# Optimization experiments

Measured on AMD Instinct MI355X. Metric: run time of the kernel, lower is better.

## Reference

```python
import jax, jax.numpy as jnp
import numpy as np

N = 100000      # nodes
E = 1600000     # edges (before self-loops)
IN = 128        # in_size
H = 4           # heads
C = 32          # out_size // heads
OUT = H * C     # 128
NEG_SLOPE = 0.2
LN_EPS = 1e-5
SM_EPS = 1e-16  # PyG softmax eps


def setup_inputs() -> dict:
    key = jax.random.key(0)
    ks = jax.random.split(key, 6)
    x = jax.random.normal(ks[0], (N, IN), dtype=jnp.float32)
    edge_index = jax.random.randint(ks[1], (2, E), 0, N, dtype=jnp.int64)
    W = jax.random.normal(ks[2], (IN, OUT), dtype=jnp.float32) * 0.05
    a_src = jax.random.normal(ks[3], (H, C), dtype=jnp.float32) * 0.05
    a_dst = jax.random.normal(ks[4], (H, C), dtype=jnp.float32) * 0.05
    bias = jnp.zeros((OUT,), dtype=jnp.float32)
    gamma = jnp.ones((OUT,), dtype=jnp.float32)
    beta = jnp.zeros((OUT,), dtype=jnp.float32)
    return {"x": x, "edge_index": edge_index, "W": W, "a_src": a_src,
            "a_dst": a_dst, "bias": bias, "gamma": gamma, "beta": beta}


def reference(x, edge_index, W, a_src, a_dst, bias, gamma, beta):
    n = x.shape[0]
    # add self loops (PyG GATConv default)
    loops = jnp.arange(n, dtype=edge_index.dtype)
    src = jnp.concatenate([edge_index[0], loops])  # [E+N]
    dst = jnp.concatenate([edge_index[1], loops])

    h = (x @ W).reshape(n, H, C)                   # [N,H,C]
    alpha_src = jnp.sum(h * a_src, axis=-1)        # [N,H]
    alpha_dst = jnp.sum(h * a_dst, axis=-1)        # [N,H]

    e = jax.nn.leaky_relu(alpha_src[src] + alpha_dst[dst], NEG_SLOPE)  # [E+N,H]
    # segment softmax over edges grouped by destination node
    emax = jax.ops.segment_max(e, dst, num_segments=n)
    emax = jnp.where(jnp.isfinite(emax), emax, 0.0)
    ee = jnp.exp(e - emax[dst])
    denom = jax.ops.segment_sum(ee, dst, num_segments=n)
    alpha = ee / (denom[dst] + SM_EPS)             # [E+N,H]

    msg = h[src] * alpha[:, :, None]               # [E+N,H,C]
    out = jax.ops.segment_sum(msg, dst, num_segments=n).reshape(n, OUT) + bias

    # LayerNorm(out_size)
    mu = jnp.mean(out, axis=-1, keepdims=True)
    var = jnp.var(out, axis=-1, keepdims=True)
    out = (out - mu) * jax.lax.rsqrt(var + LN_EPS) * gamma + beta
    return jax.nn.relu(out)
```

## Files before the change

### kernel.cpp

```cpp
#include <hip/hip_runtime.h>
#include <hip/hip_bf16.h>
#include <math.h>

#define IN_DIM 128
#define OUT_DIM 128
#define NHEAD 4
#define HC 32
#define NEG_SLOPE 0.2f
#define LN_EPS 1e-5f
#define SM_EPS 1e-16f

#define NB_SHIFT 9
#define BDST 512
#define NBUCK_MAX 256
#define BIN_ITER 28
#define BIN_CHUNK (BIN_ITER * 256)
#define SRC_BITS 17
#define SRC_MASK ((1u << SRC_BITS) - 1u)
#define BCAP_SHIFT 14
#define BCAP (1 << BCAP_SHIFT)

typedef __attribute__((ext_vector_type(8))) short bf16x8;
typedef __attribute__((ext_vector_type(4))) short short4v;
typedef __attribute__((ext_vector_type(4))) float f32x4;

__device__ __forceinline__ float leaky(float v) { return v > 0.f ? v : NEG_SLOPE * v; }

__device__ __forceinline__ short f2b(float f) {
    __hip_bfloat16 b = __float2bfloat16(f);
    return *reinterpret_cast<short*>(&b);
}

__device__ __forceinline__ int swz(int row, int byteInRow) {
    return row * 256 + (byteInRow ^ ((row & 7) << 4));
}

__global__ void k_prepW(const float* __restrict__ W, __hip_bfloat16* __restrict__ WtB)
{
    int t0 = blockIdx.x * 256 + threadIdx.x;
    int k = t0 >> 7, j = t0 & 127;
    WtB[j * IN_DIM + k] = __float2bfloat16(W[t0]);
}

__global__ void __launch_bounds__(256)
k_gemm_bin(const float* __restrict__ x, const __hip_bfloat16* __restrict__ WtB,
           const float* __restrict__ a_src, const float* __restrict__ a_dst,
           __hip_bfloat16* __restrict__ hB, float* __restrict__ asrc_out,
           float* __restrict__ adst_out,
           const int* __restrict__ ei, int* __restrict__ bcur,
           unsigned* __restrict__ binned,
           int E, int N, int nblk_gemm)
{
    __shared__ __align__(16) char lds[49152];
    const int t = threadIdx.x;

    if ((int)blockIdx.x < nblk_gemm) {
        const int node0 = blockIdx.x * 64;

        #pragma unroll
        for (int i = 0; i < 16; ++i) {
            int idx = (i * 256 + t) * 4;
            int col = idx >> 7, k = idx & 127;
            short4v w4 = *reinterpret_cast<const short4v*>((const short*)WtB + idx);
            *reinterpret_cast<short4v*>(lds + 16384 + swz(col, 2 * k)) = w4;
        }
        #pragma unroll
        for (int i = 0; i < 8; ++i) {
            int idx = (i * 256 + t) * 4;
            int row = idx >> 7, k = idx & 127;
            int node = node0 + row;
            float4 xv = make_float4(0.f, 0.f, 0.f, 0.f);
            if (node < N) xv = *reinterpret_cast<const float4*>(x + (size_t)node * IN_DIM + k);
            short4v xb = { f2b(xv.x), f2b(xv.y), f2b(xv.z), f2b(xv.w) };
            *reinterpret_cast<short4v*>(lds + swz(row, 2 * k)) = xb;
        }
        __syncthreads();

        const int wave = t >> 6, l = t & 63;
        const int lr = l & 15, lg = l >> 4;

        bf16x8 afrag[4];
        #pragma unroll
        for (int kk = 0; kk < 4; ++kk)
            afrag[kk] = *reinterpret_cast<bf16x8*>(lds + swz(wave * 16 + lr, kk * 64 + lg * 16));

        f32x4 acc[8];
        #pragma unroll
        for (int cg = 0; cg < 8; ++cg) acc[cg] = (f32x4){0.f, 0.f, 0.f, 0.f};

        #pragma unroll
        for (int cg = 0; cg < 8; ++cg) {
            #pragma unroll
            for (int kk = 0; kk < 4; ++kk) {
                bf16x8 b = *reinterpret_cast<bf16x8*>(lds + 16384 + swz(cg * 16 + lr, kk * 64 + lg * 16));
                acc[cg] = __builtin_amdgcn_mfma_f32_16x16x32_bf16(afrag[kk], b, acc[cg], 0, 0, 0);
            }
        }

        #pragma unroll
        for (int q = 0; q < 4; ++q) {
            int node = node0 + wave * 16 + lg * 4 + q;
            if (node < N) {
                #pragma unroll
                for (int cg = 0; cg < 8; ++cg)
                    hB[(size_t)node * OUT_DIM + cg * 16 + lr] = __float2bfloat16(acc[cg][q]);
            }
        }

        #pragma unroll
        for (int q = 0; q < 4; ++q) {
            int node = node0 + wave * 16 + lg * 4 + q;
            #pragma unroll
            for (int hh = 0; hh < 4; ++hh) {
                float as0 = a_src[hh * HC + lr], as1 = a_src[hh * HC + 16 + lr];
                float ad0 = a_dst[hh * HC + lr], ad1 = a_dst[hh * HC + 16 + lr];
                float s = acc[2 * hh][q] * as0 + acc[2 * hh + 1][q] * as1;
                float d = acc[2 * hh][q] * ad0 + acc[2 * hh + 1][q] * ad1;
                #pragma unroll
                for (int m = 1; m < 16; m <<= 1) {
                    s += __shfl_xor(s, m, 64);
                    d += __shfl_xor(d, m, 64);
                }
                if (lr == 0 && node < N) {
                    asrc_out[node * NHEAD + hh] = s;
                    adst_out[node * NHEAD + hh] = d;
                }
            }
        }
    } else {
        int* cnt = (int*)lds;
        int* gb  = (int*)(lds + 1024);
        int tot = E + N;
        int base = ((int)blockIdx.x - nblk_gemm) * BIN_CHUNK;

        cnt[t] = 0;
        __syncthreads();

        int rk[BIN_ITER], bk[BIN_ITER], dlo[BIN_ITER];
        #pragma unroll
        for (int k = 0; k < BIN_ITER; ++k) {
            int e = base + k * 256 + t;
            bk[k] = -1; rk[k] = 0; dlo[k] = 0;
            if (e < tot) {
                int d = (e < E) ? ei[E + e] : (e - E);
                bk[k] = d >> NB_SHIFT;
                dlo[k] = d & (BDST - 1);
                rk[k] = atomicAdd(&cnt[bk[k]], 1);
            }
        }
        __syncthreads();
        gb[t] = cnt[t] ? ((t << BCAP_SHIFT) + atomicAdd(&bcur[t], cnt[t])) : 0;
        __syncthreads();
        #pragma unroll
        for (int k = 0; k < BIN_ITER; ++k) {
            int e = base + k * 256 + t;
            if (e < tot) {
                int s = (e < E) ? ei[e] : (e - E);
                binned[gb[bk[k]] + rk[k]] = (unsigned)s | ((unsigned)dlo[k] << SRC_BITS);
            }
        }
    }
}

__global__ void k_bucket_csr(const unsigned* __restrict__ binned, const int* __restrict__ bcur,
                             int* __restrict__ rowbeg, int* __restrict__ rowend,
                             int* __restrict__ csr_src, int N)
{
    __shared__ int cnt[BDST];
    __shared__ int s2[256];
    int b = blockIdx.x;
    int t = threadIdx.x;
    int d0 = b << NB_SHIFT;
    int base = b << BCAP_SHIFT;
    int ne = bcur[b];

    cnt[t] = 0; cnt[t + 256] = 0;
    __syncthreads();
    for (int i = t; i < ne; i += 256) {
        unsigned p = binned[base + i];
        atomicAdd(&cnt[p >> SRC_BITS], 1);
    }
    __syncthreads();
    int c0 = cnt[2 * t], c1 = cnt[2 * t + 1];
    s2[t] = c0 + c1;
    __syncthreads();
    #pragma unroll
    for (int off = 1; off < 256; off <<= 1) {
        int tmp = (t >= off) ? s2[t - off] : 0;
        __syncthreads();
        s2[t] += tmp;
        __syncthreads();
    }
    int e0 = (t ? s2[t - 1] : 0);
    cnt[2 * t] = e0;
    cnt[2 * t + 1] = e0 + c0;
    if (d0 + 2 * t < N) {
        rowbeg[d0 + 2 * t] = base + e0;
        rowend[d0 + 2 * t] = base + e0 + c0;
    }
    if (d0 + 2 * t + 1 < N) {
        rowbeg[d0 + 2 * t + 1] = base + e0 + c0;
        rowend[d0 + 2 * t + 1] = base + e0 + c0 + c1;
    }
    __syncthreads();
    for (int i = t; i < ne; i += 256) {
        unsigned p = binned[base + i];
        int r = atomicAdd(&cnt[p >> SRC_BITS], 1);
        csr_src[base + r] = (int)(p & SRC_MASK);
    }
}

__global__ void k_gather(const int* __restrict__ csr_src,
                         const int* __restrict__ rowbeg, const int* __restrict__ rowend,
                         const __hip_bfloat16* __restrict__ hB,
                         const float* __restrict__ asrc, const float* __restrict__ adst,
                         const float* __restrict__ bias, const float* __restrict__ gamma,
                         const float* __restrict__ beta, float* __restrict__ out, int N)
{
    int wave = threadIdx.x >> 6;
    int l = threadIdx.x & 63;
    int d = blockIdx.x * 4 + wave;
    if (d >= N) return;
    int head = l >> 4;
    const char* hp = (const char*)hB;
    unsigned voff = (unsigned)(l << 2);
    float ad = adst[d * NHEAD + head];
    int beg = __builtin_amdgcn_readfirstlane(rowbeg[d]);
    int end = __builtin_amdgcn_readfirstlane(rowend[d]);

    float ax0 = 0.f, ay0 = 0.f, dn0 = 0.f;
    float ax1 = 0.f, ay1 = 0.f, dn1 = 0.f;

    int idx = beg + (l & 15);
    int cl = idx < end ? idx : end - 1;
    int smine = csr_src[cl];
    float v = (idx < end) ? asrc[(unsigned)smine * NHEAD + head] : -1e30f;

    for (int c = beg; c < end; c += 16) {
        float ee = __expf(leaky(v + ad));
        int scur = smine;
        int c2 = c + 16;
        if (c2 < end) {
            int idx2 = c2 + (l & 15);
            int cl2 = idx2 < end ? idx2 : end - 1;
            smine = csr_src[cl2];
            v = (idx2 < end) ? asrc[(unsigned)smine * NHEAD + head] : -1e30f;
        }

#define GLOAD(E_)                                                                     \
        unsigned se##E_ = (unsigned)__builtin_amdgcn_readlane(scur, (E_));            \
        unsigned hv##E_ = *(const unsigned*)(hp + ((size_t)se##E_ << 8) + voff);
#define GCONS(E_, AX_, AY_, DN_) {                                                    \
        float eb = __int_as_float(__builtin_amdgcn_ds_swizzle(                        \
            __float_as_int(ee), 0x10 | ((E_) << 5)));                                 \
        AX_ = fmaf(eb, __uint_as_float(hv##E_ << 16), AX_);                           \
        AY_ = fmaf(eb, __uint_as_float(hv##E_ & 0xffff0000u), AY_);  DN_ += eb;       \
    }
        { GLOAD(0) GLOAD(1) GLOAD(2) GLOAD(3) GLOAD(4) GLOAD(5) GLOAD(6) GLOAD(7)
          GCONS(0, ax0, ay0, dn0) GCONS(1, ax1, ay1, dn1)
          GCONS(2, ax0, ay0, dn0) GCONS(3, ax1, ay1, dn1)
          GCONS(4, ax0, ay0, dn0) GCONS(5, ax1, ay1, dn1)
          GCONS(6, ax0, ay0, dn0) GCONS(7, ax1, ay1, dn1) }
        { GLOAD(8) GLOAD(9) GLOAD(10) GLOAD(11) GLOAD(12) GLOAD(13) GLOAD(14) GLOAD(15)
          GCONS(8, ax0, ay0, dn0)  GCONS(9, ax1, ay1, dn1)
          GCONS(10, ax0, ay0, dn0) GCONS(11, ax1, ay1, dn1)
          GCONS(12, ax0, ay0, dn0) GCONS(13, ax1, ay1, dn1)
          GCONS(14, ax0, ay0, dn0) GCONS(15, ax1, ay1, dn1) }
#undef GLOAD
#undef GCONS
    }

    float accx = ax0 + ax1, accy = ay0 + ay1, den = dn0 + dn1;
    float inv = 1.f / (den + SM_EPS);
    float vx = accx * inv + bias[2 * l];
    float vy = accy * inv + bias[2 * l + 1];

    float s1 = vx + vy;
    float s2 = vx * vx + vy * vy;
    #pragma unroll
    for (int m = 32; m >= 1; m >>= 1) {
        s1 += __shfl_xor(s1, m, 64);
        s2 += __shfl_xor(s2, m, 64);
    }
    float mean = s1 * (1.f / OUT_DIM);
    float var = s2 * (1.f / OUT_DIM) - mean * mean;
    float r = rsqrtf(var + LN_EPS);
    float ox = (vx - mean) * r * gamma[2 * l] + beta[2 * l];
    float oy = (vy - mean) * r * gamma[2 * l + 1] + beta[2 * l + 1];
    ox = ox > 0.f ? ox : 0.f;
    oy = oy > 0.f ? oy : 0.f;
    *reinterpret_cast<float2*>(&out[(size_t)d * OUT_DIM + 2 * l]) = make_float2(ox, oy);
}

extern "C" void kernel_launch(void* const* d_in, const int* in_sizes, int n_in,
                              void* d_out, int out_size, void* d_ws, size_t ws_size,
                              hipStream_t stream) {
    const float* x      = (const float*)d_in[0];
    const int*   ei     = (const int*)d_in[1];
    const float* W      = (const float*)d_in[2];
    const float* a_src  = (const float*)d_in[3];
    const float* a_dst  = (const float*)d_in[4];
    const float* bias   = (const float*)d_in[5];
    const float* gamma  = (const float*)d_in[6];
    const float* beta   = (const float*)d_in[7];
    float* out = (float*)d_out;

    const int N = in_sizes[0] / IN_DIM;
    const int E = in_sizes[1] / 2;
    const int TOT = E + N;
    const int nbuck = (N + BDST - 1) >> NB_SHIFT;
    const int nblk_gemm = (N + 63) / 64;
    const int nblk_bin = (TOT + BIN_CHUNK - 1) / BIN_CHUNK;

    char* p = (char*)d_ws;
    __hip_bfloat16* hB = (__hip_bfloat16*)p;  p += (size_t)N * OUT_DIM * sizeof(__hip_bfloat16);
    __hip_bfloat16* WtB = (__hip_bfloat16*)p; p += (size_t)IN_DIM * OUT_DIM * sizeof(__hip_bfloat16);
    float* asrc   = (float*)p;                p += (size_t)N * NHEAD * sizeof(float);
    float* adst   = (float*)p;                p += (size_t)N * NHEAD * sizeof(float);
    int* bcur     = (int*)p;                  p += NBUCK_MAX * sizeof(int);
    int* rowbeg   = (int*)p;                  p += (size_t)N * sizeof(int);
    int* rowend   = (int*)p;                  p += (size_t)N * sizeof(int);
    unsigned* binned = (unsigned*)p;          p += (size_t)nbuck * BCAP * sizeof(unsigned);
    int* csr_src  = (int*)p;                  p += (size_t)nbuck * BCAP * sizeof(int);

    (void)hipMemsetAsync(bcur, 0, NBUCK_MAX * sizeof(int), stream);

    k_prepW<<<64, 256, 0, stream>>>(W, WtB);
    k_gemm_bin<<<nblk_gemm + nblk_bin, 256, 0, stream>>>(x, WtB, a_src, a_dst, hB, asrc, adst,
                                                         ei, bcur, binned, E, N, nblk_gemm);
    k_bucket_csr<<<nbuck, 256, 0, stream>>>(binned, bcur, rowbeg, rowend, csr_src, N);
    k_gather<<<(N + 3) / 4, 256, 0, stream>>>(csr_src, rowbeg, rowend, hB, asrc, adst,
                                              bias, gamma, beta, out, N);
}
```

Baseline: 161.6 us.

## Split GEMM from binning, stage hB stores via LDS, compute alpha from hB

The fused GEMM+binning kernel is split in two. The GEMM kernel now writes its output tile through LDS so each thread stores full 16-byte rows to hB, instead of scattered 2-byte stores. The attention logits are no longer reduced with shuffles in the GEMM epilogue; a separate grid-stride section inside the binning kernel re-reads hB and computes them. This adds a kernel launch and an extra read of hB, and gives up the overlap of binning with the GEMM, in exchange for coalesced stores and a lighter GEMM epilogue.

```diff
diff --git a/kernel.cpp b/kernel.cpp
--- a/kernel.cpp
+++ b/kernel.cpp
@@ -43,95 +43,92 @@
 }
 
 __global__ void __launch_bounds__(256)
-k_gemm_bin(const float* __restrict__ x, const __hip_bfloat16* __restrict__ WtB,
-           const float* __restrict__ a_src, const float* __restrict__ a_dst,
-           __hip_bfloat16* __restrict__ hB, float* __restrict__ asrc_out,
-           float* __restrict__ adst_out,
-           const int* __restrict__ ei, int* __restrict__ bcur,
-           unsigned* __restrict__ binned,
-           int E, int N, int nblk_gemm)
+k_gemm(const float* __restrict__ x, const __hip_bfloat16* __restrict__ WtB,
+       __hip_bfloat16* __restrict__ hB, int N)
 {
     __shared__ __align__(16) char lds[49152];
     const int t = threadIdx.x;
-
-    if ((int)blockIdx.x < nblk_gemm) {
-        const int node0 = blockIdx.x * 64;
-
-        #pragma unroll
-        for (int i = 0; i < 16; ++i) {
-            int idx = (i * 256 + t) * 4;
-            int col = idx >> 7, k = idx & 127;
-            short4v w4 = *reinterpret_cast<const short4v*>((const short*)WtB + idx);
-            *reinterpret_cast<short4v*>(lds + 16384 + swz(col, 2 * k)) = w4;
-        }
-        #pragma unroll
-        for (int i = 0; i < 8; ++i) {
-            int idx = (i * 256 + t) * 4;
-            int row = idx >> 7, k = idx & 127;
-            int node = node0 + row;
-            float4 xv = make_float4(0.f, 0.f, 0.f, 0.f);
-            if (node < N) xv = *reinterpret_cast<const float4*>(x + (size_t)node * IN_DIM + k);
-            short4v xb = { f2b(xv.x), f2b(xv.y), f2b(xv.z), f2b(xv.w) };
-            *reinterpret_cast<short4v*>(lds + swz(row, 2 * k)) = xb;
-        }
-        __syncthreads();
-
-        const int wave = t >> 6, l = t & 63;
-        const int lr = l & 15, lg = l >> 4;
-
-        bf16x8 afrag[4];
-        #pragma unroll
-        for (int kk = 0; kk < 4; ++kk)
-            afrag[kk] = *reinterpret_cast<bf16x8*>(lds + swz(wave * 16 + lr, kk * 64 + lg * 16));
-
-        f32x4 acc[8];
-        #pragma unroll
-        for (int cg = 0; cg < 8; ++cg) acc[cg] = (f32x4){0.f, 0.f, 0.f, 0.f};
-
-        #pragma unroll
-        for (int cg = 0; cg < 8; ++cg) {
+    const int node0 = blockIdx.x * 64;
+
+    #pragma unroll
+    for (int i = 0; i < 16; ++i) {
+        int idx = (i * 256 + t) * 4;
+        int col = idx >> 7, k = idx & 127;
+        short4v w4 = *reinterpret_cast<const short4v*>((const short*)WtB + idx);
+        *reinterpret_cast<short4v*>(lds + 16384 + swz(col, 2 * k)) = w4;
+    }
+    #pragma unroll
+    for (int i = 0; i < 8; ++i) {
+        int idx = (i * 256 + t) * 4;
+        int row = idx >> 7, k = idx & 127;
+        int node = node0 + row;
+        float4 xv = make_float4(0.f, 0.f, 0.f, 0.f);
+        if (node < N) xv = *reinterpret_cast<const float4*>(x + (size_t)node * IN_DIM + k);
+        short4v xb = { f2b(xv.x), f2b(xv.y), f2b(xv.z), f2b(xv.w) };
+        *reinterpret_cast<short4v*>(lds + swz(row, 2 * k)) = xb;
+    }
+    __syncthreads();
+
+    const int wave = t >> 6, l = t & 63;
+    const int lr = l & 15, lg = l >> 4;
+
+    bf16x8 afrag[4];
+    #pragma unroll
+    for (int kk = 0; kk < 4; ++kk)
+        afrag[kk] = *reinterpret_cast<bf16x8*>(lds + swz(wave * 16 + lr, kk * 64 + lg * 16));
+
+    f32x4 acc[8];
+    #pragma unroll
+    for (int cg = 0; cg < 8; ++cg) acc[cg] = (f32x4){0.f, 0.f, 0.f, 0.f};
+
+    #pragma unroll
+    for (int cg = 0; cg < 8; ++cg) {
+        #pragma unroll
+        for (int kk = 0; kk < 4; ++kk) {
+            bf16x8 b = *reinterpret_cast<bf16x8*>(lds + 16384 + swz(cg * 16 + lr, kk * 64 + lg * 16));
+            acc[cg] = __builtin_amdgcn_mfma_f32_16x16x32_bf16(afrag[kk], b, acc[cg], 0, 0, 0);
+        }
+    }
+
+    __syncthreads();
+    #pragma unroll
+    for (int q = 0; q < 4; ++q) {
+        int row = wave * 16 + lg * 4 + q;
+        #pragma unroll
+        for (int cg = 0; cg < 8; ++cg)
+            *reinterpret_cast<short*>(lds + swz(row, (cg * 16 + lr) * 2)) = f2b(acc[cg][q]);
+    }
+    __syncthreads();
+
+    {
+        int row = t >> 2;
+        int node = node0 + row;
+        if (node < N) {
+            char* dst = (char*)(hB + (size_t)node * OUT_DIM);
             #pragma unroll
-            for (int kk = 0; kk < 4; ++kk) {
-                bf16x8 b = *reinterpret_cast<bf16x8*>(lds + 16384 + swz(cg * 16 + lr, kk * 64 + lg * 16));
-                acc[cg] = __builtin_amdgcn_mfma_f32_16x16x32_bf16(afrag[kk], b, acc[cg], 0, 0, 0);
-            }
-        }
-
-        #pragma unroll
-        for (int q = 0; q < 4; ++q) {
-            int node = node0 + wave * 16 + lg * 4 + q;
-            if (node < N) {
-                #pragma unroll
-                for (int cg = 0; cg < 8; ++cg)
-                    hB[(size_t)node * OUT_DIM + cg * 16 + lr] = __float2bfloat16(acc[cg][q]);
-            }
-        }
-
-        #pragma unroll
-        for (int q = 0; q < 4; ++q) {
-            int node = node0 + wave * 16 + lg * 4 + q;
-            #pragma unroll
-            for (int hh = 0; hh < 4; ++hh) {
-                float as0 = a_src[hh * HC + lr], as1 = a_src[hh * HC + 16 + lr];
-                float ad0 = a_dst[hh * HC + lr], ad1 = a_dst[hh * HC + 16 + lr];
-                float s = acc[2 * hh][q] * as0 + acc[2 * hh + 1][q] * as1;
-                float d = acc[2 * hh][q] * ad0 + acc[2 * hh + 1][q] * ad1;
-                #pragma unroll
-                for (int m = 1; m < 16; m <<= 1) {
-                    s += __shfl_xor(s, m, 64);
-                    d += __shfl_xor(d, m, 64);
-                }
-                if (lr == 0 && node < N) {
-                    asrc_out[node * NHEAD + hh] = s;
-                    adst_out[node * NHEAD + hh] = d;
-                }
-            }
-        }
-    } else {
-        int* cnt = (int*)lds;
-        int* gb  = (int*)(lds + 1024);
+            for (int c = 0; c < 4; ++c) {
+                int bir = (t & 3) * 64 + c * 16;
+                bf16x8 vv = *reinterpret_cast<bf16x8*>(lds + swz(row, bir));
+                *reinterpret_cast<bf16x8*>(dst + bir) = vv;
+            }
+        }
+    }
+}
+
+__global__ void __launch_bounds__(256)
+k_bin_alpha(const int* __restrict__ ei, int* __restrict__ bcur, unsigned* __restrict__ binned,
+            const __hip_bfloat16* __restrict__ hB,
+            const float* __restrict__ a_src, const float* __restrict__ a_dst,
+            float* __restrict__ asrc_out, float* __restrict__ adst_out,
+            int E, int N, int nblk_bin, int nblk_alpha)
+{
+    __shared__ int cnt[NBUCK_MAX];
+    __shared__ int gb[NBUCK_MAX];
+    int t = threadIdx.x;
+
+    if ((int)blockIdx.x < nblk_bin) {
         int tot = E + N;
-        int base = ((int)blockIdx.x - nblk_gemm) * BIN_CHUNK;
+        int base = (int)blockIdx.x * BIN_CHUNK;
 
         cnt[t] = 0;
         __syncthreads();
@@ -157,6 +154,35 @@
             if (e < tot) {
                 int s = (e < E) ? ei[e] : (e - E);
                 binned[gb[bk[k]] + rk[k]] = (unsigned)s | ((unsigned)dlo[k] << SRC_BITS);
+            }
+        }
+    } else {
+        int l = t & 63, wave = t >> 6;
+        int li = l & 15, sub = l >> 4;
+        int head = li >> 2;
+        float as[8], ad[8];
+        #pragma unroll
+        for (int j = 0; j < 8; ++j) { as[j] = a_src[li * 8 + j]; ad[j] = a_dst[li * 8 + j]; }
+
+        int blk = (int)blockIdx.x - nblk_bin;
+        for (int nb = blk * 16; nb < N; nb += nblk_alpha * 16) {
+            int node = nb + wave * 4 + sub;
+            float s = 0.f, d = 0.f;
+            if (node < N) {
+                bf16x8 hb = *reinterpret_cast<const bf16x8*>(
+                    (const short*)hB + (size_t)node * OUT_DIM + li * 8);
+                #pragma unroll
+                for (int j = 0; j < 8; ++j) {
+                    float hf = __uint_as_float(((unsigned)(unsigned short)hb[j]) << 16);
+                    s = fmaf(hf, as[j], s);
+                    d = fmaf(hf, ad[j], d);
+                }
+            }
+            s += __shfl_xor(s, 1, 64); s += __shfl_xor(s, 2, 64);
+            d += __shfl_xor(d, 1, 64); d += __shfl_xor(d, 2, 64);
+            if ((li & 3) == 0 && node < N) {
+                asrc_out[node * NHEAD + head] = s;
+                adst_out[node * NHEAD + head] = d;
             }
         }
     }
@@ -311,6 +337,7 @@
     const int nbuck = (N + BDST - 1) >> NB_SHIFT;
     const int nblk_gemm = (N + 63) / 64;
     const int nblk_bin = (TOT + BIN_CHUNK - 1) / BIN_CHUNK;
+    const int nblk_alpha = 256;
 
     char* p = (char*)d_ws;
     __hip_bfloat16* hB = (__hip_bfloat16*)p;  p += (size_t)N * OUT_DIM * sizeof(__hip_bfloat16);
@@ -326,8 +353,9 @@
     (void)hipMemsetAsync(bcur, 0, NBUCK_MAX * sizeof(int), stream);
 
     k_prepW<<<64, 256, 0, stream>>>(W, WtB);
-    k_gemm_bin<<<nblk_gemm + nblk_bin, 256, 0, stream>>>(x, WtB, a_src, a_dst, hB, asrc, adst,
-                                                         ei, bcur, binned, E, N, nblk_gemm);
+    k_gemm<<<nblk_gemm, 256, 0, stream>>>(x, WtB, hB, N);
+    k_bin_alpha<<<nblk_bin + nblk_alpha, 256, 0, stream>>>(ei, bcur, binned, hB, a_src, a_dst,
+                                                           asrc, adst, E, N, nblk_bin, nblk_alpha);
     k_bucket_csr<<<nbuck, 256, 0, stream>>>(binned, bcur, rowbeg, rowend, csr_src, N);
     k_gather<<<(N + 3) / 4, 256, 0, stream>>>(csr_src, rowbeg, rowend, hB, asrc, adst,
                                               bias, gamma, beta, out, N);
```

Result: no change. 163.0 us (+0.8%).

## Stage GEMM output through LDS for coalesced stores and fold memset into prepW

Applied to the files above, without the earlier changes.

The GEMM epilogue now writes bf16 accumulators into swizzled LDS, then each thread copies a 64-byte head slice of one node row with 16-byte vector stores and computes that head's attention logits from the bf16 values. This replaces the scattered 2-byte global stores and the shuffle reductions. The bucket-counter memset is also folded into the weight-prep kernel to remove one API launch. The logits are now computed from bf16-rounded h rather than fp32 accumulators, which slightly changes numerics.

```diff
diff --git a/kernel.cpp b/kernel.cpp
--- a/kernel.cpp
+++ b/kernel.cpp
@@ -30,16 +30,21 @@
     __hip_bfloat16 b = __float2bfloat16(f);
     return *reinterpret_cast<short*>(&b);
 }
+__device__ __forceinline__ float b2f(short s) {
+    return __uint_as_float(((unsigned)(unsigned short)s) << 16);
+}
 
 __device__ __forceinline__ int swz(int row, int byteInRow) {
     return row * 256 + (byteInRow ^ ((row & 7) << 4));
 }
 
-__global__ void k_prepW(const float* __restrict__ W, __hip_bfloat16* __restrict__ WtB)
+__global__ void k_prepW(const float* __restrict__ W, __hip_bfloat16* __restrict__ WtB,
+                        int* __restrict__ bcur)
 {
     int t0 = blockIdx.x * 256 + threadIdx.x;
     int k = t0 >> 7, j = t0 & 127;
     WtB[j * IN_DIM + k] = __float2bfloat16(W[t0]);
+    if (blockIdx.x == 0) bcur[threadIdx.x] = 0;
 }
 
 __global__ void __launch_bounds__(256)
@@ -97,34 +102,37 @@
             }
         }
 
+        __syncthreads();
         #pragma unroll
         for (int q = 0; q < 4; ++q) {
-            int node = node0 + wave * 16 + lg * 4 + q;
+            int row = wave * 16 + lg * 4 + q;
+            #pragma unroll
+            for (int cg = 0; cg < 8; ++cg)
+                *reinterpret_cast<short*>(lds + swz(row, (cg * 16 + lr) * 2)) = f2b(acc[cg][q]);
+        }
+        __syncthreads();
+
+        {
+            int row = t >> 2;
+            int node = node0 + row;
+            int head = t & 3;
             if (node < N) {
+                char* dst = (char*)(hB + (size_t)node * OUT_DIM);
+                float s = 0.f, dd = 0.f;
                 #pragma unroll
-                for (int cg = 0; cg < 8; ++cg)
-                    hB[(size_t)node * OUT_DIM + cg * 16 + lr] = __float2bfloat16(acc[cg][q]);
-            }
-        }
-
-        #pragma unroll
-        for (int q = 0; q < 4; ++q) {
-            int node = node0 + wave * 16 + lg * 4 + q;
-            #pragma unroll
-            for (int hh = 0; hh < 4; ++hh) {
-                float as0 = a_src[hh * HC + lr], as1 = a_src[hh * HC + 16 + lr];
-                float ad0 = a_dst[hh * HC + lr], ad1 = a_dst[hh * HC + 16 + lr];
-                float s = acc[2 * hh][q] * as0 + acc[2 * hh + 1][q] * as1;
-                float d = acc[2 * hh][q] * ad0 + acc[2 * hh + 1][q] * ad1;
-                #pragma unroll
-                for (int m = 1; m < 16; m <<= 1) {
-                    s += __shfl_xor(s, m, 64);
-                    d += __shfl_xor(d, m, 64);
+                for (int c = 0; c < 4; ++c) {
+                    int bir = head * 64 + c * 16;
+                    bf16x8 vv = *reinterpret_cast<bf16x8*>(lds + swz(row, bir));
+                    *reinterpret_cast<bf16x8*>(dst + bir) = vv;
+                    #pragma unroll
+                    for (int j = 0; j < 8; ++j) {
+                        float hf = b2f(vv[j]);
+                        s  = fmaf(hf, a_src[head * HC + c * 8 + j], s);
+                        dd = fmaf(hf, a_dst[head * HC + c * 8 + j], dd);
+                    }
                 }
-                if (lr == 0 && node < N) {
-                    asrc_out[node * NHEAD + hh] = s;
-                    adst_out[node * NHEAD + hh] = d;
-                }
+                asrc_out[node * NHEAD + head] = s;
+                adst_out[node * NHEAD + head] = dd;
             }
         }
     } else {
@@ -323,9 +331,7 @@
     unsigned* binned = (unsigned*)p;          p += (size_t)nbuck * BCAP * sizeof(unsigned);
     int* csr_src  = (int*)p;                  p += (size_t)nbuck * BCAP * sizeof(int);
 
-    (void)hipMemsetAsync(bcur, 0, NBUCK_MAX * sizeof(int), stream);
-
-    k_prepW<<<64, 256, 0, stream>>>(W, WtB);
+    k_prepW<<<64, 256, 0, stream>>>(W, WtB, bcur);
     k_gemm_bin<<<nblk_gemm + nblk_bin, 256, 0, stream>>>(x, WtB, a_src, a_dst, hB, asrc, adst,
                                                          ei, bcur, binned, E, N, nblk_gemm);
     k_bucket_csr<<<nbuck, 256, 0, stream>>>(binned, bcur, rowbeg, rowend, csr_src, N);
```

Result: no change. 159.3 us (-1.4%).
